# Kernel tuning notes

Measured on AMD Instinct MI355X. Metric: run time of the kernel, lower is better.

Reference implementation:

```python
import jax, jax.numpy as jnp
import numpy as np
from jax import lax

B, L, C = 128, 200, 300          # batch, text_len, embed_channels
K = 128                          # conv_num_kernel
WS = (2, 3, 4, 5)                # conv_kernel_size
A = 5000                         # num_api
F = 64                           # feature_channels


def setup_inputs() -> dict:
    key = jax.random.key(0)
    ks = jax.random.split(key, 24)
    s = 0.02
    inp = {"x": jax.random.normal(ks[0], (B, L, C), dtype=jnp.float32)}
    for i, ws in enumerate(WS):
        inp[f"conv_w{ws}"] = jax.random.normal(ks[1 + i], (K, C, ws), dtype=jnp.float32) * s
        inp[f"conv_b{ws}"] = jnp.zeros((K,), dtype=jnp.float32)
    D = K * len(WS)
    inp["sc_fcl_w"] = jax.random.normal(ks[5], (A, D), dtype=jnp.float32) * s
    inp["sc_fcl_b"] = jnp.zeros((A,), dtype=jnp.float32)
    inp["fic_fc_w"] = jax.random.normal(ks[6], (F, D), dtype=jnp.float32) * s
    inp["fic_fc_b"] = jnp.zeros((F,), dtype=jnp.float32)
    inp["emb"] = jax.random.uniform(ks[7], (F, A), dtype=jnp.float32)  # torch.rand
    inp["mlp_w1"] = jax.random.normal(ks[8], (F, 2 * F), dtype=jnp.float32) * s
    inp["mlp_b1"] = jnp.zeros((F,), dtype=jnp.float32)
    inp["mlp_w2"] = jax.random.normal(ks[9], (1, F), dtype=jnp.float32) * s
    inp["mlp_b2"] = jnp.zeros((1,), dtype=jnp.float32)
    inp["fic_fcl_w"] = jax.random.normal(ks[10], (A, 2 * A), dtype=jnp.float32) * s
    inp["fic_fcl_b"] = jnp.zeros((A,), dtype=jnp.float32)
    inp["fusion_w"] = jax.random.normal(ks[11], (A, 2 * A), dtype=jnp.float32) * s
    inp["fusion_b"] = jnp.zeros((A,), dtype=jnp.float32)
    inp["task_w"] = jax.random.normal(ks[12], (A, A), dtype=jnp.float32) * s
    inp["task_b"] = jnp.zeros((A,), dtype=jnp.float32)
    return inp


def _textcnn(x_t, conv_ws, conv_bs):
    # x_t: (B, C, L); each branch: conv1d VALID -> relu -> global max over width -> (B, K)
    feats = []
    for w, b in zip(conv_ws, conv_bs):
        y = lax.conv_general_dilated(x_t, w, (1,), 'VALID',
                                     dimension_numbers=('NCH', 'OIH', 'NCH'))
        y = jax.nn.relu(y + b[None, :, None])
        feats.append(jnp.max(y, axis=2))  # full-width max-pool -> (B, K)
    # torch: cat along width dim=2 of (B,K,1) then view(B,-1) -> kernel-window index fastest
    return jnp.stack(feats, axis=2).reshape(x_t.shape[0], -1)  # (B, K*len(WS))


def reference(x, conv_w2, conv_b2, conv_w3, conv_b3, conv_w4, conv_b4,
              conv_w5, conv_b5, sc_fcl_w, sc_fcl_b, fic_fc_w, fic_fc_b, emb,
              mlp_w1, mlp_b1, mlp_w2, mlp_b2, fic_fcl_w, fic_fcl_b,
              fusion_w, fusion_b, task_w, task_b):
    x_t = jnp.transpose(x, (0, 2, 1))  # (B, C, L)
    e = _textcnn(x_t, (conv_w2, conv_w3, conv_w4, conv_w5),
                 (conv_b2, conv_b3, conv_b4, conv_b5))  # (B, D)

    u_sc = e @ sc_fcl_w.T + sc_fcl_b          # (B, A)
    u_sc_trans = e @ fic_fc_w.T + fic_fc_b    # (B, F)
    u_mm = u_sc_trans @ emb                   # (B, A)

    # Batched form of the per-sample repeat/concat + MLP loop:
    # concat(u_rep, emb.T) @ W1.T  ==  u @ W1[:, :F].T (bcast over A) + emb.T @ W1[:, F:].T
    h = (u_sc_trans @ mlp_w1[:, :F].T)[:, None, :] \
        + (emb.T @ mlp_w1[:, F:].T)[None, :, :] + mlp_b1  # (B, A, F)
    u_mlp = jnp.tanh(jnp.einsum('baf,f->ba', h, mlp_w2[0]) + mlp_b2[0])  # (B, A)

    u_fic = jnp.tanh(jnp.concatenate([u_mm, u_mlp], axis=1) @ fic_fcl_w.T + fic_fcl_b)
    u_mmf = jnp.concatenate([u_sc, u_fic], axis=1) @ fusion_w.T + fusion_b
    task = u_mmf @ task_w.T + task_b          # (B, A)
    return task
```

## Files before the change

### kernel.cpp

```cpp
#include <hip/hip_runtime.h>
#include <math.h>

#define B_ 128
#define L_ 200
#define C_ 300
#define K_ 128
#define A_ 5000
#define F_ 64
#define D_ 512
#define CP_ 320
#define LP_ 260
#define NPAD_ 5056
#define KP2_ 10048
#define KP1_ 5056

typedef __attribute__((ext_vector_type(8))) short bf16x8;
typedef __attribute__((ext_vector_type(8))) short short8;
typedef __attribute__((ext_vector_type(4))) float f32x4;

#define MFMA(a,b,c) __builtin_amdgcn_mfma_f32_16x16x32_bf16(a,b,c,0,0,0)

#define ROFF(r) ((r)*32 + ((r)>>2)*8)

static __device__ __forceinline__ unsigned short f2bf(float f) {
    unsigned u = __float_as_uint(f);
    unsigned r = (u + 0x7FFFu + ((u >> 16) & 1u)) >> 16;
    return (unsigned short)r;
}

#define OFF_XP     ((size_t)0)
#define OFF_WP     ((size_t)5324800)
#define OFF_E      ((size_t)5611520)
#define OFF_EBF    ((size_t)5677056)
#define OFF_UST    ((size_t)5693440)
#define OFF_VB     ((size_t)5701632)
#define OFF_S2     ((size_t)5701696)
#define OFF_UMBF   ((size_t)5701824)
#define OFF_UFBF   ((size_t)6344896)
#define OFF_UMMFBF ((size_t)6987968)
#define OFF_PART   ((size_t)7311552)

__global__ __launch_bounds__(320) void prep_x_kernel(const float* __restrict__ x, short* __restrict__ xp)
{
    const int row = blockIdx.x;
    const int b   = blockIdx.y;
    const int c   = threadIdx.x;
    float v = 0.f;
    if (row < L_ && c < C_) v = x[((size_t)b * L_ + row) * C_ + c];
    xp[((size_t)b * LP_ + row) * CP_ + c] = (short)f2bf(v);
}

__global__ void prep_w_kernel(const float* __restrict__ w2, const float* __restrict__ w3,
                              const float* __restrict__ w4, const float* __restrict__ w5,
                              short* __restrict__ wp)
{
    const int idx = blockIdx.x * 256 + threadIdx.x;
    if (idx >= 128 * 14 * CP_) return;
    int off, wsz; const float* src;
    if (idx < 81920)       { off = idx;          wsz = 2; src = w2; }
    else if (idx < 204800) { off = idx - 81920;  wsz = 3; src = w3; }
    else if (idx < 368640) { off = idx - 204800; wsz = 4; src = w4; }
    else                   { off = idx - 368640; wsz = 5; src = w5; }
    const int k   = off / (wsz * CP_);
    const int r   = off % (wsz * CP_);
    const int tap = r / CP_;
    const int c   = r % CP_;
    float v = 0.f;
    if (c < C_) v = src[((size_t)k * C_ + c) * wsz + tap];
    wp[idx] = (short)f2bf(v);
}

template<int WSZ>
__device__ __forceinline__ void conv_body(
    const short* __restrict__ xbase, const short* __restrict__ wpb,
    const float* __restrict__ bp, float* __restrict__ e, short* __restrict__ ebf,
    int b, int br, short* lA, short* lB, float (*smax)[128])
{
    const int Pout = 199 - br;
    const int tid  = threadIdx.x;
    const int wave = tid >> 6;
    const int lane = tid & 63;
    const int mw   = wave & 1;
    const int nw   = wave >> 1;

    f32x4 acc[8][4];
    #pragma unroll
    for (int mf = 0; mf < 8; ++mf)
        #pragma unroll
        for (int nf = 0; nf < 4; ++nf)
            acc[mf][nf] = (f32x4){0.f, 0.f, 0.f, 0.f};

    short8 aR[5];
    short8 bR[2 * WSZ];

    #define LDA4(ch, cc) (*(const short8*)(xbase + (size_t)((ch) >> 2) * CP_ + (cc) * 32 + ((ch) & 3) * 8))
    #define LDB4(ch, cc) (*(const short8*)(wpb + (size_t)(((ch) >> 2) & 127) * (WSZ * CP_) + (((ch) >> 2) >> 7) * CP_ + (cc) * 32 + ((ch) & 3) * 8))

    #pragma unroll
    for (int k = 0; k < 5; ++k) {
        const int ch = tid + k * 256;
        if (k < 4 || ch < 1040) aR[k] = LDA4(ch, 0);
    }
    #pragma unroll
    for (int k = 0; k < 2 * WSZ; ++k) bR[k] = LDB4(tid + k * 256, 0);

    for (int cc = 0; cc < 10; ++cc) {
        __syncthreads();
        #pragma unroll
        for (int k = 0; k < 5; ++k) {
            const int ch = tid + k * 256;
            if (k < 4 || ch < 1040)
                *(short8*)(lA + ROFF(ch >> 2) + (ch & 3) * 8) = aR[k];
        }
        #pragma unroll
        for (int k = 0; k < 2 * WSZ; ++k) {
            const int ch = tid + k * 256;
            *(short8*)(lB + ROFF(ch >> 2) + (ch & 3) * 8) = bR[k];
        }
        __syncthreads();
        if (cc + 1 < 10) {
            #pragma unroll
            for (int k = 0; k < 5; ++k) {
                const int ch = tid + k * 256;
                if (k < 4 || ch < 1040) aR[k] = LDA4(ch, cc + 1);
            }
            #pragma unroll
            for (int k = 0; k < 2 * WSZ; ++k) bR[k] = LDB4(tid + k * 256, cc + 1);
        }
        #pragma unroll
        for (int tap = 0; tap < WSZ; ++tap) {
            bf16x8 bfr[4];
            #pragma unroll
            for (int nf = 0; nf < 4; ++nf)
                bfr[nf] = *(const bf16x8*)(lB + ROFF(tap * 128 + nw * 64 + nf * 16 + (lane & 15)) + (lane >> 4) * 8);
            #pragma unroll
            for (int mf = 0; mf < 8; ++mf) {
                const bf16x8 af = *(const bf16x8*)(lA + ROFF(mw * 128 + mf * 16 + (lane & 15) + tap) + (lane >> 4) * 8);
                #pragma unroll
                for (int nf = 0; nf < 4; ++nf)
                    acc[mf][nf] = MFMA(af, bfr[nf], acc[mf][nf]);
            }
        }
    }
    #undef LDA4
    #undef LDB4

    float vm[4] = {-1e30f, -1e30f, -1e30f, -1e30f};
    #pragma unroll
    for (int mf = 0; mf < 8; ++mf) {
        const int rowbase = mw * 128 + mf * 16 + (lane >> 4) * 4;
        #pragma unroll
        for (int r = 0; r < 4; ++r) {
            const bool valid = (rowbase + r) < Pout;
            #pragma unroll
            for (int nf = 0; nf < 4; ++nf)
                vm[nf] = fmaxf(vm[nf], valid ? acc[mf][nf][r] : -1e30f);
        }
    }
    #pragma unroll
    for (int nf = 0; nf < 4; ++nf) {
        vm[nf] = fmaxf(vm[nf], __shfl_xor(vm[nf], 16));
        vm[nf] = fmaxf(vm[nf], __shfl_xor(vm[nf], 32));
    }
    if (lane < 16) {
        #pragma unroll
        for (int nf = 0; nf < 4; ++nf)
            smax[mw][nw * 64 + nf * 16 + lane] = vm[nf];
    }
    __syncthreads();
    if (tid < 128) {
        const float m = fmaxf(smax[0][tid], smax[1][tid]);
        const float val = fmaxf(bp[tid] + m, 0.f);
        e[(size_t)b * D_ + tid * 4 + br] = val;
        ebf[(size_t)b * D_ + tid * 4 + br] = (short)f2bf(val);
    }
}

__global__ __launch_bounds__(256) void conv_gemm4_kernel(
    const short* __restrict__ xp, const short* __restrict__ wp,
    const float* __restrict__ b2, const float* __restrict__ b3,
    const float* __restrict__ b4, const float* __restrict__ b5,
    float* __restrict__ e, short* __restrict__ ebf)
{
    __shared__ short lA[8832];
    __shared__ short lB[21752];
    __shared__ float smax[2][128];

    const int b  = blockIdx.x;
    const int br = blockIdx.y;
    const short* xbase = xp + (size_t)b * LP_ * CP_;

    if (br == 0)      conv_body<2>(xbase, wp,          b2, e, ebf, b, 0, lA, lB, smax);
    else if (br == 1) conv_body<3>(xbase, wp + 81920,  b3, e, ebf, b, 1, lA, lB, smax);
    else if (br == 2) conv_body<4>(xbase, wp + 204800, b4, e, ebf, b, 2, lA, lB, smax);
    else              conv_body<5>(xbase, wp + 368640, b5, e, ebf, b, 3, lA, lB, smax);
}

__global__ __launch_bounds__(512) void gemm3_kernel(
    const short* __restrict__ Abf, int Kpad,
    const float* __restrict__ W, int K, int N,
    int steps_per_z, float* __restrict__ partial)
{
    const int n0 = blockIdx.x * 64;
    const int total = Kpad >> 6;
    const int sbeg = blockIdx.y * steps_per_z;
    const int send = min(sbeg + steps_per_z, total);

    const int tid  = threadIdx.x;
    const int wave = tid >> 6;
    const int lane = tid & 63;
    const int mw   = wave & 3;
    const int nw   = wave >> 2;

    __shared__ short lA[128 * 68];
    __shared__ short lB[64 * 68];

    const int arow = tid >> 2, ac0 = (tid & 3) * 16;
    const int fil  = tid >> 3, wc0 = (tid & 7) * 8;

    f32x4 acc[2][2];
    #pragma unroll
    for (int mf = 0; mf < 2; ++mf)
        #pragma unroll
        for (int nf = 0; nf < 2; ++nf)
            acc[mf][nf] = (f32x4){0.f, 0.f, 0.f, 0.f};

    short8 ra0, ra1;
    float4 rw0, rw1;
    const bool wrow_ok = (n0 + fil) < N;

    {
        const int kb = sbeg * 64;
        ra0 = *(const short8*)(Abf + (size_t)arow * Kpad + kb + ac0);
        ra1 = *(const short8*)(Abf + (size_t)arow * Kpad + kb + ac0 + 8);
        rw0 = make_float4(0.f,0.f,0.f,0.f); rw1 = rw0;
        if (wrow_ok && (kb + wc0) < K)     rw0 = *(const float4*)(W + (size_t)(n0 + fil) * K + kb + wc0);
        if (wrow_ok && (kb + wc0 + 4) < K) rw1 = *(const float4*)(W + (size_t)(n0 + fil) * K + kb + wc0 + 4);
    }

    for (int s = sbeg; s < send; ++s) {
        __syncthreads();
        *(short8*)(lA + arow * 68 + ac0)     = ra0;
        *(short8*)(lA + arow * 68 + ac0 + 8) = ra1;
        {
            short8 wb;
            wb[0]=(short)f2bf(rw0.x); wb[1]=(short)f2bf(rw0.y); wb[2]=(short)f2bf(rw0.z); wb[3]=(short)f2bf(rw0.w);
            wb[4]=(short)f2bf(rw1.x); wb[5]=(short)f2bf(rw1.y); wb[6]=(short)f2bf(rw1.z); wb[7]=(short)f2bf(rw1.w);
            *(short8*)(lB + fil * 68 + wc0) = wb;
        }
        __syncthreads();
        if (s + 1 < send) {
            const int kb = (s + 1) * 64;
            ra0 = *(const short8*)(Abf + (size_t)arow * Kpad + kb + ac0);
            ra1 = *(const short8*)(Abf + (size_t)arow * Kpad + kb + ac0 + 8);
            float4 t0 = make_float4(0.f,0.f,0.f,0.f), t1 = t0;
            if (wrow_ok && (kb + wc0) < K)     t0 = *(const float4*)(W + (size_t)(n0 + fil) * K + kb + wc0);
            if (wrow_ok && (kb + wc0 + 4) < K) t1 = *(const float4*)(W + (size_t)(n0 + fil) * K + kb + wc0 + 4);
            rw0 = t0; rw1 = t1;
        }
        #pragma unroll
        for (int ks = 0; ks < 2; ++ks) {
            bf16x8 af[2], bfr[2];
            #pragma unroll
            for (int mf = 0; mf < 2; ++mf)
                af[mf] = *(const bf16x8*)(lA + (mw * 32 + mf * 16 + (lane & 15)) * 68 + ks * 32 + (lane >> 4) * 8);
            #pragma unroll
            for (int nf = 0; nf < 2; ++nf)
                bfr[nf] = *(const bf16x8*)(lB + (nw * 32 + nf * 16 + (lane & 15)) * 68 + ks * 32 + (lane >> 4) * 8);
            #pragma unroll
            for (int mf = 0; mf < 2; ++mf)
                #pragma unroll
                for (int nf = 0; nf < 2; ++nf)
                    acc[mf][nf] = MFMA(af[mf], bfr[nf], acc[mf][nf]);
        }
    }

    #pragma unroll
    for (int mf = 0; mf < 2; ++mf)
        #pragma unroll
        for (int nf = 0; nf < 2; ++nf)
            #pragma unroll
            for (int r = 0; r < 4; ++r) {
                const int row = mw * 32 + mf * 16 + (lane >> 4) * 4 + r;
                const int col = nw * 32 + nf * 16 + (lane & 15);
                partial[((size_t)blockIdx.y * B_ + row) * NPAD_ + n0 + col] = acc[mf][nf][r];
            }
}

__global__ void reduce2_kernel(const float* __restrict__ partial, const float* __restrict__ bias,
                               float* __restrict__ outf, short* __restrict__ outb,
                               int N, int ldo, int ooff, int js, int act, int padn)
{
    const int Ntot = N + padn;
    const int idx = blockIdx.x * 256 + threadIdx.x;
    if (idx >= B_ * Ntot) return;
    const int n = idx % Ntot;
    const int b = idx / Ntot;
    if (n >= N) { outb[(size_t)b * ldo + ooff + n] = 0; return; }
    float s = bias[n];
    for (int k = 0; k < js; ++k) s += partial[((size_t)k * B_ + b) * NPAD_ + n];
    if (act) s = tanhf(s);
    if (outb) outb[(size_t)b * ldo + ooff + n] = (short)f2bf(s);
    else      outf[(size_t)b * ldo + ooff + n] = s;
}

__global__ __launch_bounds__(256) void ust_kernel(
    const float* __restrict__ e, const float* __restrict__ W,
    const float* __restrict__ bias, float* __restrict__ ust)
{
    const int b = blockIdx.x;
    const int f = threadIdx.x >> 2;
    const int q = threadIdx.x & 3;
    const float* er = e + (size_t)b * D_ + q * 128;
    const float* wr = W + (size_t)f * D_ + q * 128;
    float acc = 0.f;
    #pragma unroll
    for (int j = 0; j < 128; j += 4) {
        const float4 ev = *(const float4*)(er + j);
        const float4 wv = *(const float4*)(wr + j);
        acc += ev.x*wv.x + ev.y*wv.y + ev.z*wv.z + ev.w*wv.w;
    }
    acc += __shfl_xor(acc, 1);
    acc += __shfl_xor(acc, 2);
    if (q == 0) ust[(size_t)b * F_ + f] = acc + bias[f];
}

__global__ void prep_kernel(const float* __restrict__ mlp_w1, const float* __restrict__ mlp_b1,
                            const float* __restrict__ mlp_w2, const float* __restrict__ mlp_b2,
                            const float* __restrict__ ust,
                            float* __restrict__ vB, float* __restrict__ s2)
{
    __shared__ float vA[64];
    __shared__ float csh;
    const int tid = threadIdx.x;
    if (tid < 64) {
        float a = 0.f;
        for (int f = 0; f < 64; ++f) a += mlp_w2[f] * mlp_w1[f * 128 + tid];
        vA[tid] = a;
    } else {
        const int g = tid - 64;
        float bsum = 0.f;
        for (int f = 0; f < 64; ++f) bsum += mlp_w2[f] * mlp_w1[f * 128 + 64 + g];
        vB[g] = bsum;
    }
    if (tid == 0) {
        float c = mlp_b2[0];
        for (int f = 0; f < 64; ++f) c += mlp_b1[f] * mlp_w2[f];
        csh = c;
    }
    __syncthreads();
    float s = csh;
    const float* ub = ust + (size_t)tid * F_;
    for (int g = 0; g < 64; ++g) s += ub[g] * vA[g];
    s2[tid] = s;
}

__global__ void um3_kernel(const float* __restrict__ ust, const float* __restrict__ emb,
                           const float* __restrict__ s2, const float* __restrict__ vB,
                           short* __restrict__ umb)
{
    const int b = blockIdx.y;
    __shared__ float us[64];
    __shared__ float vb[64];
    if (threadIdx.x < 64) {
        us[threadIdx.x] = ust[(size_t)b * F_ + threadIdx.x];
        vb[threadIdx.x] = vB[threadIdx.x];
    }
    __syncthreads();
    const int a = blockIdx.x * 256 + threadIdx.x;
    if (a < A_) {
        float accm = 0.f, acct = 0.f;
        #pragma unroll
        for (int g = 0; g < 64; ++g) {
            const float ev = emb[(size_t)g * A_ + a];
            accm += us[g] * ev;
            acct += vb[g] * ev;
        }
        umb[(size_t)b * KP2_ + a] = (short)f2bf(accm);
        umb[(size_t)b * KP2_ + A_ + a] = (short)f2bf(tanhf(s2[b] + acct));
    } else if (a < A_ + 48) {
        umb[(size_t)b * KP2_ + A_ + a] = 0;
    }
}

extern "C" void kernel_launch(void* const* d_in, const int* in_sizes, int n_in,
                              void* d_out, int out_size, void* d_ws, size_t ws_size,
                              hipStream_t stream)
{
    const float* x       = (const float*)d_in[0];
    const float* conv_w2 = (const float*)d_in[1];
    const float* conv_b2 = (const float*)d_in[2];
    const float* conv_w3 = (const float*)d_in[3];
    const float* conv_b3 = (const float*)d_in[4];
    const float* conv_w4 = (const float*)d_in[5];
    const float* conv_b4 = (const float*)d_in[6];
    const float* conv_w5 = (const float*)d_in[7];
    const float* conv_b5 = (const float*)d_in[8];
    const float* sc_fcl_w = (const float*)d_in[9];
    const float* sc_fcl_b = (const float*)d_in[10];
    const float* fic_fc_w = (const float*)d_in[11];
    const float* fic_fc_b = (const float*)d_in[12];
    const float* emb      = (const float*)d_in[13];
    const float* mlp_w1   = (const float*)d_in[14];
    const float* mlp_b1   = (const float*)d_in[15];
    const float* mlp_w2   = (const float*)d_in[16];
    const float* mlp_b2   = (const float*)d_in[17];
    const float* fic_fcl_w = (const float*)d_in[18];
    const float* fic_fcl_b = (const float*)d_in[19];
    const float* fusion_w  = (const float*)d_in[20];
    const float* fusion_b  = (const float*)d_in[21];
    const float* task_w    = (const float*)d_in[22];
    const float* task_b    = (const float*)d_in[23];

    float* ws = (float*)d_ws;
    short* xp     = (short*)(ws + OFF_XP);
    short* wp     = (short*)(ws + OFF_WP);
    float* e      = ws + OFF_E;
    short* ebf    = (short*)(ws + OFF_EBF);
    float* ust    = ws + OFF_UST;
    float* vB     = ws + OFF_VB;
    float* s2     = ws + OFF_S2;
    short* umbf   = (short*)(ws + OFF_UMBF);
    short* ufbf   = (short*)(ws + OFF_UFBF);
    short* ummfbf = (short*)(ws + OFF_UMMFBF);
    float* part   = ws + OFF_PART;
    float* out    = (float*)d_out;

    prep_x_kernel<<<dim3(LP_, B_), CP_, 0, stream>>>(x, xp);
    prep_w_kernel<<<(128*14*CP_ + 255)/256, 256, 0, stream>>>(conv_w2, conv_w3, conv_w4, conv_w5, wp);

    conv_gemm4_kernel<<<dim3(B_, 4), 256, 0, stream>>>(xp, wp, conv_b2, conv_b3, conv_b4, conv_b5, e, ebf);

    gemm3_kernel<<<dim3(79, 4), 512, 0, stream>>>(ebf, D_, sc_fcl_w, D_, A_, 2, part);
    reduce2_kernel<<<(B_*A_ + 255)/256, 256, 0, stream>>>(part, sc_fcl_b, nullptr, ufbf, A_, KP2_, 0, 4, 0, 0);

    ust_kernel<<<B_, 256, 0, stream>>>(e, fic_fc_w, fic_fc_b, ust);

    prep_kernel<<<1, 128, 0, stream>>>(mlp_w1, mlp_b1, mlp_w2, mlp_b2, ust, vB, s2);
    um3_kernel<<<dim3(20, B_), 256, 0, stream>>>(ust, emb, s2, vB, umbf);

    gemm3_kernel<<<dim3(79, 12), 512, 0, stream>>>(umbf, KP2_, fic_fcl_w, 2*A_, A_, 14, part);
    reduce2_kernel<<<(B_*(A_+48) + 255)/256, 256, 0, stream>>>(part, fic_fcl_b, nullptr, ufbf, A_, KP2_, A_, 12, 1, 48);

    gemm3_kernel<<<dim3(79, 12), 512, 0, stream>>>(ufbf, KP2_, fusion_w, 2*A_, A_, 14, part);
    reduce2_kernel<<<(B_*(A_+56) + 255)/256, 256, 0, stream>>>(part, fusion_b, nullptr, ummfbf, A_, KP1_, 0, 12, 0, 56);

    gemm3_kernel<<<dim3(79, 12), 512, 0, stream>>>(ummfbf, KP1_, task_w, A_, A_, 7, part);
    reduce2_kernel<<<(B_*A_ + 255)/256, 256, 0, stream>>>(part, task_b, out, nullptr, A_, A_, 0, 12, 0, 0);
}
```

Measured before the change: 317.6 us.

## Double-buffer LDS and deepen global prefetch in split-K GEMM

Measured after the change: 502.3 us. 1.58x slower.

```diff
diff --git a/kernel.cpp b/kernel.cpp
--- a/kernel.cpp
+++ b/kernel.cpp
@@ -196,7 +196,9 @@
     else              conv_body<5>(xbase, wp + 368640, b5, e, ebf, b, 3, lA, lB, smax);
 }
 
-__global__ __launch_bounds__(512) void gemm3_kernel(
+#define LDSHALF 13056
+
+__global__ __launch_bounds__(512) void gemm4_kernel(
     const short* __restrict__ Abf, int Kpad,
     const float* __restrict__ W, int K, int N,
     int steps_per_z, float* __restrict__ partial)
@@ -205,6 +207,8 @@
     const int total = Kpad >> 6;
     const int sbeg = blockIdx.y * steps_per_z;
     const int send = min(sbeg + steps_per_z, total);
+    const int ns   = send - sbeg;
+    const int nslast = ns - 1;
 
     const int tid  = threadIdx.x;
     const int wave = tid >> 6;
@@ -212,11 +216,13 @@
     const int mw   = wave & 3;
     const int nw   = wave >> 2;
 
-    __shared__ short lA[128 * 68];
-    __shared__ short lB[64 * 68];
+    __shared__ short lds[2 * LDSHALF];
 
     const int arow = tid >> 2, ac0 = (tid & 3) * 16;
     const int fil  = tid >> 3, wc0 = (tid & 7) * 8;
+    const int wrow = (n0 + fil < N) ? (n0 + fil) : (N - 1);
+    const float* Wr = W + (size_t)wrow * K;
+    const short* Ar = Abf + (size_t)arow * Kpad;
 
     f32x4 acc[2][2];
     #pragma unroll
@@ -225,55 +231,83 @@
         for (int nf = 0; nf < 2; ++nf)
             acc[mf][nf] = (f32x4){0.f, 0.f, 0.f, 0.f};
 
-    short8 ra0, ra1;
-    float4 rw0, rw1;
-    const bool wrow_ok = (n0 + fil) < N;
-
-    {
-        const int kb = sbeg * 64;
-        ra0 = *(const short8*)(Abf + (size_t)arow * Kpad + kb + ac0);
-        ra1 = *(const short8*)(Abf + (size_t)arow * Kpad + kb + ac0 + 8);
-        rw0 = make_float4(0.f,0.f,0.f,0.f); rw1 = rw0;
-        if (wrow_ok && (kb + wc0) < K)     rw0 = *(const float4*)(W + (size_t)(n0 + fil) * K + kb + wc0);
-        if (wrow_ok && (kb + wc0 + 4) < K) rw1 = *(const float4*)(W + (size_t)(n0 + fil) * K + kb + wc0 + 4);
-    }
-
-    for (int s = sbeg; s < send; ++s) {
-        __syncthreads();
-        *(short8*)(lA + arow * 68 + ac0)     = ra0;
-        *(short8*)(lA + arow * 68 + ac0 + 8) = ra1;
-        {
-            short8 wb;
-            wb[0]=(short)f2bf(rw0.x); wb[1]=(short)f2bf(rw0.y); wb[2]=(short)f2bf(rw0.z); wb[3]=(short)f2bf(rw0.w);
-            wb[4]=(short)f2bf(rw1.x); wb[5]=(short)f2bf(rw1.y); wb[6]=(short)f2bf(rw1.z); wb[7]=(short)f2bf(rw1.w);
-            *(short8*)(lB + fil * 68 + wc0) = wb;
-        }
-        __syncthreads();
-        if (s + 1 < send) {
-            const int kb = (s + 1) * 64;
-            ra0 = *(const short8*)(Abf + (size_t)arow * Kpad + kb + ac0);
-            ra1 = *(const short8*)(Abf + (size_t)arow * Kpad + kb + ac0 + 8);
-            float4 t0 = make_float4(0.f,0.f,0.f,0.f), t1 = t0;
-            if (wrow_ok && (kb + wc0) < K)     t0 = *(const float4*)(W + (size_t)(n0 + fil) * K + kb + wc0);
-            if (wrow_ok && (kb + wc0 + 4) < K) t1 = *(const float4*)(W + (size_t)(n0 + fil) * K + kb + wc0 + 4);
-            rw0 = t0; rw1 = t1;
-        }
-        #pragma unroll
-        for (int ks = 0; ks < 2; ++ks) {
-            bf16x8 af[2], bfr[2];
-            #pragma unroll
-            for (int mf = 0; mf < 2; ++mf)
-                af[mf] = *(const bf16x8*)(lA + (mw * 32 + mf * 16 + (lane & 15)) * 68 + ks * 32 + (lane >> 4) * 8);
-            #pragma unroll
-            for (int nf = 0; nf < 2; ++nf)
-                bfr[nf] = *(const bf16x8*)(lB + (nw * 32 + nf * 16 + (lane & 15)) * 68 + ks * 32 + (lane >> 4) * 8);
-            #pragma unroll
-            for (int mf = 0; mf < 2; ++mf)
-                #pragma unroll
-                for (int nf = 0; nf < 2; ++nf)
-                    acc[mf][nf] = MFMA(af[mf], bfr[nf], acc[mf][nf]);
-        }
-    }
+    short8 rA0a, rA0b, rA1a, rA1b;
+    float4 rW0a, rW0b, rW1a, rW1b;
+
+    #define GISSUE(slot, t) do { \
+        const int kb_ = (sbeg + (t)) * 64; \
+        rA##slot##a = *(const short8*)(Ar + kb_ + ac0); \
+        rA##slot##b = *(const short8*)(Ar + kb_ + ac0 + 8); \
+        int k1_ = kb_ + wc0;     if (k1_ >= K) k1_ = 0; \
+        int k2_ = kb_ + wc0 + 4; if (k2_ >= K) k2_ = 0; \
+        rW##slot##a = *(const float4*)(Wr + k1_); \
+        rW##slot##b = *(const float4*)(Wr + k2_); \
+    } while (0)
+
+    #define STORE(slot, bufi) do { \
+        short* lA_ = lds + (bufi) * LDSHALF; \
+        short* lB_ = lA_ + 128 * 68; \
+        *(short8*)(lA_ + arow * 68 + ac0)     = rA##slot##a; \
+        *(short8*)(lA_ + arow * 68 + ac0 + 8) = rA##slot##b; \
+        short8 wb_; \
+        wb_[0]=(short)f2bf(rW##slot##a.x); wb_[1]=(short)f2bf(rW##slot##a.y); \
+        wb_[2]=(short)f2bf(rW##slot##a.z); wb_[3]=(short)f2bf(rW##slot##a.w); \
+        wb_[4]=(short)f2bf(rW##slot##b.x); wb_[5]=(short)f2bf(rW##slot##b.y); \
+        wb_[6]=(short)f2bf(rW##slot##b.z); wb_[7]=(short)f2bf(rW##slot##b.w); \
+        *(short8*)(lB_ + fil * 68 + wc0) = wb_; \
+    } while (0)
+
+    #define COMPUTE(bufi) do { \
+        const short* lA_ = lds + (bufi) * LDSHALF; \
+        const short* lB_ = lA_ + 128 * 68; \
+        _Pragma("unroll") \
+        for (int ks = 0; ks < 2; ++ks) { \
+            bf16x8 af[2], bfr[2]; \
+            _Pragma("unroll") \
+            for (int mf = 0; mf < 2; ++mf) \
+                af[mf] = *(const bf16x8*)(lA_ + (mw * 32 + mf * 16 + (lane & 15)) * 68 + ks * 32 + (lane >> 4) * 8); \
+            _Pragma("unroll") \
+            for (int nf = 0; nf < 2; ++nf) \
+                bfr[nf] = *(const bf16x8*)(lB_ + (nw * 32 + nf * 16 + (lane & 15)) * 68 + ks * 32 + (lane >> 4) * 8); \
+            _Pragma("unroll") \
+            for (int mf = 0; mf < 2; ++mf) \
+                _Pragma("unroll") \
+                for (int nf = 0; nf < 2; ++nf) \
+                    acc[mf][nf] = MFMA(af[mf], bfr[nf], acc[mf][nf]); \
+        } \
+    } while (0)
+
+    #define STEP(s, CUR, NXT) do { \
+        asm volatile("s_waitcnt vmcnt(4)" ::: "memory"); \
+        STORE(NXT, NXT); \
+        { int tt_ = (s) + 3; if (tt_ > nslast) tt_ = nslast; GISSUE(NXT, tt_); } \
+        COMPUTE(CUR); \
+        asm volatile("s_waitcnt lgkmcnt(0)" ::: "memory"); \
+        __builtin_amdgcn_s_barrier(); \
+        asm volatile("" ::: "memory"); \
+    } while (0)
+
+    GISSUE(0, 0);
+    { int t1_ = (1 > nslast) ? nslast : 1; GISSUE(1, t1_); }
+    asm volatile("s_waitcnt vmcnt(4)" ::: "memory");
+    STORE(0, 0);
+    { int t2_ = (2 > nslast) ? nslast : 2; GISSUE(0, t2_); }
+    asm volatile("s_waitcnt lgkmcnt(0)" ::: "memory");
+    __builtin_amdgcn_s_barrier();
+    asm volatile("" ::: "memory");
+
+    int s = 0;
+    while (s + 1 < ns) {
+        STEP(s,     0, 1);
+        STEP(s + 1, 1, 0);
+        s += 2;
+    }
+    if (s < ns) STEP(s, 0, 1);
+
+    #undef GISSUE
+    #undef STORE
+    #undef COMPUTE
+    #undef STEP
 
     #pragma unroll
     for (int mf = 0; mf < 2; ++mf)
@@ -431,7 +465,7 @@
 
     conv_gemm4_kernel<<<dim3(B_, 4), 256, 0, stream>>>(xp, wp, conv_b2, conv_b3, conv_b4, conv_b5, e, ebf);
 
-    gemm3_kernel<<<dim3(79, 4), 512, 0, stream>>>(ebf, D_, sc_fcl_w, D_, A_, 2, part);
+    gemm4_kernel<<<dim3(79, 4), 512, 0, stream>>>(ebf, D_, sc_fcl_w, D_, A_, 2, part);
     reduce2_kernel<<<(B_*A_ + 255)/256, 256, 0, stream>>>(part, sc_fcl_b, nullptr, ufbf, A_, KP2_, 0, 4, 0, 0);
 
     ust_kernel<<<B_, 256, 0, stream>>>(e, fic_fc_w, fic_fc_b, ust);
@@ -439,12 +473,12 @@
     prep_kernel<<<1, 128, 0, stream>>>(mlp_w1, mlp_b1, mlp_w2, mlp_b2, ust, vB, s2);
     um3_kernel<<<dim3(20, B_), 256, 0, stream>>>(ust, emb, s2, vB, umbf);
 
-    gemm3_kernel<<<dim3(79, 12), 512, 0, stream>>>(umbf, KP2_, fic_fcl_w, 2*A_, A_, 14, part);
+    gemm4_kernel<<<dim3(79, 12), 512, 0, stream>>>(umbf, KP2_, fic_fcl_w, 2*A_, A_, 14, part);
     reduce2_kernel<<<(B_*(A_+48) + 255)/256, 256, 0, stream>>>(part, fic_fcl_b, nullptr, ufbf, A_, KP2_, A_, 12, 1, 48);
 
-    gemm3_kernel<<<dim3(79, 12), 512, 0, stream>>>(ufbf, KP2_, fusion_w, 2*A_, A_, 14, part);
+    gemm4_kernel<<<dim3(79, 12), 512, 0, stream>>>(ufbf, KP2_, fusion_w, 2*A_, A_, 14, part);
     reduce2_kernel<<<(B_*(A_+56) + 255)/256, 256, 0, stream>>>(part, fusion_b, nullptr, ummfbf, A_, KP1_, 0, 12, 0, 56);
 
-    gemm3_kernel<<<dim3(79, 12), 512, 0, stream>>>(ummfbf, KP1_, task_w, A_, A_, 7, part);
+    gemm4_kernel<<<dim3(79, 12), 512, 0, stream>>>(ummfbf, KP1_, task_w, A_, A_, 7, part);
     reduce2_kernel<<<(B_*A_ + 255)/256, 256, 0, stream>>>(part, task_b, out, nullptr, A_, A_, 0, 12, 0, 0);
 }
```
